# Kernel optimization log

Measured on AMD Instinct MI355X. Metric: run time of the kernel, lower is better.

## Reference

```python
import jax, jax.numpy as jnp
import numpy as np

B = 256      # number of graphs (args.batch_size)
NPG = 1000   # nodes per graph (args.num_node)
C = 64       # in_channels
DEG = 16     # avg degree
K = 500      # ceil(ratio * NPG), ratio = 0.5
EPS = 1e-8


def setup_inputs() -> dict:
    key = jax.random.key(0)
    k1, k2, k3, k4, k5 = jax.random.split(key, 5)
    N = B * NPG
    epg = NPG * DEG  # edges per graph
    x = jax.random.normal(k1, (N, C), jnp.float32)
    src = jax.random.randint(k2, (B, epg), 0, NPG)
    dst = jax.random.randint(k3, (B, epg), 0, NPG)
    off = (jnp.arange(B, dtype=jnp.int32) * NPG)[:, None]
    edge_index = jnp.stack([(src + off).reshape(-1), (dst + off).reshape(-1)]).astype(jnp.int32)
    edge_attr = jax.random.uniform(k4, (B * epg,), jnp.float32)
    batch = jnp.repeat(jnp.arange(B, dtype=jnp.int32), NPG)
    W = jax.random.normal(k5, (C, C), jnp.float32) * (1.0 / np.sqrt(C))
    b = jnp.zeros((C,), jnp.float32)
    return {"istraining": 1, "x": x, "edge_index": edge_index, "edge_attr": edge_attr,
            "batch": batch, "W": W, "b": b}


def _gcn_conv(x, edge_index, W, b):
    # PyG GCNConv: x' = D^{-1/2} (A + I) D^{-1/2} X W + b, unit edge weights.
    N = x.shape[0]
    sl = jnp.arange(N, dtype=edge_index.dtype)
    src = jnp.concatenate([edge_index[0], sl])  # message source j
    dst = jnp.concatenate([edge_index[1], sl])  # aggregation target i
    deg = jnp.zeros((N,), x.dtype).at[dst].add(1.0)
    dinv = jnp.where(deg > 0, jax.lax.rsqrt(jnp.maximum(deg, 1.0)), 0.0)
    norm = dinv[src] * dinv[dst]          # [E+N]
    h = x @ W                              # [N, C]
    msg = h[src] * norm[:, None]           # gather + scale (dominant traffic)
    out = jax.ops.segment_sum(msg, dst, num_segments=N) + b
    return out


def _node_score(x):
    # compute_node_score: cosine similarity of each node to its graph centroid
    # (community prototype), plus KL(softmax(score) || uniform) per graph.
    xb = x.reshape(B, NPG, C)
    cen = xb.mean(axis=1, keepdims=True)                       # [B,1,C]
    num = jnp.sum(xb * cen, axis=-1)                           # [B,NPG]
    den = jnp.linalg.norm(xb, axis=-1) * jnp.linalg.norm(cen, axis=-1) + EPS
    score = num / den                                          # [B,NPG]
    logp = jax.nn.log_softmax(score, axis=1)
    kl = jnp.sum(jnp.exp(logp) * (logp + jnp.log(jnp.float32(NPG))), axis=1)  # [B]
    indices_ = jnp.argsort(-score, axis=1)                     # [B,NPG]
    return score, kl, indices_


def reference(istraining, x, edge_index, edge_attr, batch, W, b):
    N = x.shape[0]
    x = _gcn_conv(x, edge_index, W, b)
    score, kl_all_batch, indices_ = _node_score(x)
    # per-graph top-k (fixed k since every graph has NPG nodes)
    _, idx = jax.lax.top_k(score, K)                           # [B,K]
    perm = ((jnp.arange(B, dtype=idx.dtype) * NPG)[:, None] + idx).reshape(-1)  # [B*K]
    score_flat = score.reshape(-1)
    x_new = x[perm] * jnp.tanh(score_flat[perm])[:, None]
    batch_new = batch[perm]
    # filter_adj: keep edges with both endpoints retained, re-index to new ids.
    mapping = jnp.full((N,), -1, dtype=jnp.int32).at[perm].set(
        jnp.arange(perm.shape[0], dtype=jnp.int32))
    new_ei = mapping[edge_index]                               # [2,E], -1 = dropped
    edge_mask = jnp.logical_and(new_ei[0] >= 0, new_ei[1] >= 0)
    edge_attr_new = jnp.where(edge_mask, edge_attr, 0.0)
    return (x_new, new_ei, edge_attr_new, edge_mask, batch_new, perm, kl_all_batch, indices_)
```

## Files before the change

### kernel.cpp

```cpp
#include <hip/hip_runtime.h>
#include <math.h>

#define NPG 1000
#define KTOP 500
#define C 64
#define EPG 16000
#define BPG 63

__device__ __forceinline__ float readlane_f(float v, int l) {
    return __uint_as_float(__builtin_amdgcn_readlane(__float_as_uint(v), (unsigned)l));
}
__device__ __forceinline__ int readlane_i(int v, int l) {
    return (int)__builtin_amdgcn_readlane((unsigned)v, (unsigned)l);
}

__global__ __launch_bounds__(1024) void build_graph_k(const int* __restrict__ ei, int E,
                                                      int* __restrict__ deg,
                                                      float* __restrict__ dinv,
                                                      int* __restrict__ off,
                                                      int* __restrict__ csr) {
    int g = blockIdx.x, t = threadIdx.x;
    __shared__ int cnt[NPG];
    __shared__ int soff[NPG];
    __shared__ unsigned short lcsr[EPG];
    __shared__ int red[1024];
    const int gbase = g * NPG;
    const int ebase = g * EPG;
    const int* __restrict__ srcp = ei + ebase;
    const int* __restrict__ dstp = ei + E + ebase;

    for (int i = t; i < NPG; i += 1024) cnt[i] = 0;
    __syncthreads();
    for (int i = t; i < EPG; i += 1024) atomicAdd(&cnt[dstp[i] - gbase], 1);
    __syncthreads();
    int v = (t < NPG) ? cnt[t] : 0;
    red[t] = v;
    __syncthreads();
    for (int o = 1; o < 1024; o <<= 1) {
        int xx = (t >= o) ? red[t - o] : 0;
        __syncthreads();
        red[t] += xx;
        __syncthreads();
    }
    if (t < NPG) soff[t] = red[t] - v;
    __syncthreads();
    for (int i = t; i < NPG; i += 1024) {
        int d = cnt[i];
        deg[gbase + i] = d;
        dinv[gbase + i] = 1.0f / sqrtf((float)(d + 1));
        off[gbase + i] = ebase + soff[i];
    }
    __syncthreads();
    for (int i = t; i < NPG; i += 1024) cnt[i] = soff[i];
    __syncthreads();
    for (int i = t; i < EPG; i += 1024) {
        int d = dstp[i] - gbase;
        int pos = atomicAdd(&cnt[d], 1);
        lcsr[pos] = (unsigned short)(srcp[i] - gbase);
    }
    __syncthreads();
    int4* co = (int4*)(csr + ebase);
    for (int i = t; i < EPG / 4; i += 1024) {
        int4 vv;
        vv.x = gbase + (int)lcsr[i * 4 + 0];
        vv.y = gbase + (int)lcsr[i * 4 + 1];
        vv.z = gbase + (int)lcsr[i * 4 + 2];
        vv.w = gbase + (int)lcsr[i * 4 + 3];
        co[i] = vv;
    }
}

__global__ __launch_bounds__(256) void gemm_k(const float* __restrict__ x,
                                              const float* __restrict__ W,
                                              const float* __restrict__ dinv,
                                              float* __restrict__ h2, int N) {
    __shared__ float sW[C * C];
    int t = threadIdx.x;
    for (int i = t; i < C * C / 4; i += 256) ((float4*)sW)[i] = ((const float4*)W)[i];
    __syncthreads();
    int r0 = blockIdx.x * 512 + t;
    int r1 = r0 + 256;
    if (r0 >= N) return;
    bool has1 = (r1 < N);
    const float4* x0 = (const float4*)(x + (size_t)r0 * C);
    const float4* x1 = (const float4*)(x + (size_t)(has1 ? r1 : r0) * C);
    float acc0[C], acc1[C];
#pragma unroll
    for (int i = 0; i < C; ++i) { acc0[i] = 0.f; acc1[i] = 0.f; }
    float4 a0 = x0[0], a1 = x1[0];
    for (int k4 = 0; k4 < 16; ++k4) {
        float4 b0, b1;
        if (k4 < 15) { b0 = x0[k4 + 1]; b1 = x1[k4 + 1]; }
        const float4* wr = (const float4*)(sW + k4 * 4 * C);
        const float* a0f = (const float*)&a0;
        const float* a1f = (const float*)&a1;
#pragma unroll
        for (int c4 = 0; c4 < 16; ++c4) {
            float4 w[4];
            w[0] = wr[c4]; w[1] = wr[16 + c4]; w[2] = wr[32 + c4]; w[3] = wr[48 + c4];
            const float* wf = (const float*)w;
#pragma unroll
            for (int j = 0; j < 4; ++j) {
                float s0 = acc0[c4 * 4 + j], s1 = acc1[c4 * 4 + j];
#pragma unroll
                for (int kk = 0; kk < 4; ++kk) {
                    float wv = wf[kk * 4 + j];
                    s0 = fmaf(a0f[kk], wv, s0);
                    s1 = fmaf(a1f[kk], wv, s1);
                }
                acc0[c4 * 4 + j] = s0; acc1[c4 * 4 + j] = s1;
            }
        }
        a0 = b0; a1 = b1;
    }
    float dv0 = dinv[r0];
    float dv1 = has1 ? dinv[r1] : 0.f;
#pragma unroll
    for (int i = 0; i < C; ++i) { acc0[i] *= dv0; acc1[i] *= dv1; }
    float4* h0 = (float4*)(h2 + (size_t)r0 * C);
#pragma unroll
    for (int q = 0; q < 16; ++q) h0[q] = ((float4*)acc0)[q];
    if (has1) {
        float4* h1 = (float4*)(h2 + (size_t)r1 * C);
#pragma unroll
        for (int q = 0; q < 16; ++q) h1[q] = ((float4*)acc1)[q];
    }
}

__global__ __launch_bounds__(256) void gather_k(const int* __restrict__ csr,
                                                const int* __restrict__ off,
                                                const int* __restrict__ deg,
                                                const float* __restrict__ h2,
                                                const float* __restrict__ dinv,
                                                const float* __restrict__ bias,
                                                float* __restrict__ out2,
                                                float* __restrict__ cen_sum,
                                                int N, int B) {
    __shared__ float cenacc[C];
    int blk = blockIdx.x;
    int wave = threadIdx.x >> 6;
    int lane = threadIdx.x & 63;
    int t = threadIdx.x;
    int g, blkin;
    if ((B & 7) == 0) {
        int xcd = blk & 7, slot = blk >> 3;
        g = (slot / BPG) * 8 + xcd;
        blkin = slot % BPG;
    } else {
        g = blk / BPG;
        blkin = blk % BPG;
    }
    if (t < C) cenacc[t] = 0.f;
    __syncthreads();

    int base = blkin * 4 + wave;
    bool active = (base < NPG / 4);
    if (active) {
        int nA = g * NPG + base;
        int nB = nA + 250, nC = nA + 500, nD = nA + 750;
        int oA = off[nA], oB = off[nB], oC = off[nC], oD = off[nD];
        int dA = deg[nA], dB = deg[nB], dC = deg[nC], dD = deg[nD];
        float diA = dinv[nA], diB = dinv[nB], diC = dinv[nC], diD = dinv[nD];
        float hA = h2[(size_t)nA * C + lane];
        float hB = h2[(size_t)nB * C + lane];
        float hC = h2[(size_t)nC * C + lane];
        float hD = h2[(size_t)nD * C + lane];
        float bv = bias[lane];
        int svA = (lane < dA) ? csr[oA + lane] : nA;
        int svB = (lane < dB) ? csr[oB + lane] : nB;
        int svC = (lane < dC) ? csr[oC + lane] : nC;
        int svD = (lane < dD) ? csr[oD + lane] : nD;
        int jmA = dA < 64 ? dA : 64;
        int jmB = dB < 64 ? dB : 64;
        int jmC = dC < 64 ? dC : 64;
        int jmD = dD < 64 ? dD : 64;
        int rA = (jmA + 3) & ~3, rB = (jmB + 3) & ~3;
        int rC = (jmC + 3) & ~3, rD = (jmD + 3) & ~3;
        int m0 = rA > rB ? rA : rB;
        int m1 = rC > rD ? rC : rD;
        int mmax = m0 > m1 ? m0 : m1;
        float aA = 0.f, aB = 0.f, aC = 0.f, aD = 0.f;
        for (int j = 0; j < mmax; j += 4) {
            if (j < rA) {
                int s0 = readlane_i(svA, j + 0), s1 = readlane_i(svA, j + 1);
                int s2 = readlane_i(svA, j + 2), s3 = readlane_i(svA, j + 3);
                float v0 = h2[(size_t)s0 * C + lane];
                float v1 = h2[(size_t)s1 * C + lane];
                float v2 = h2[(size_t)s2 * C + lane];
                float v3 = h2[(size_t)s3 * C + lane];
                aA += (v0 + v1) + (v2 + v3);
            }
            if (j < rB) {
                int s0 = readlane_i(svB, j + 0), s1 = readlane_i(svB, j + 1);
                int s2 = readlane_i(svB, j + 2), s3 = readlane_i(svB, j + 3);
                float v0 = h2[(size_t)s0 * C + lane];
                float v1 = h2[(size_t)s1 * C + lane];
                float v2 = h2[(size_t)s2 * C + lane];
                float v3 = h2[(size_t)s3 * C + lane];
                aB += (v0 + v1) + (v2 + v3);
            }
            if (j < rC) {
                int s0 = readlane_i(svC, j + 0), s1 = readlane_i(svC, j + 1);
                int s2 = readlane_i(svC, j + 2), s3 = readlane_i(svC, j + 3);
                float v0 = h2[(size_t)s0 * C + lane];
                float v1 = h2[(size_t)s1 * C + lane];
                float v2 = h2[(size_t)s2 * C + lane];
                float v3 = h2[(size_t)s3 * C + lane];
                aC += (v0 + v1) + (v2 + v3);
            }
            if (j < rD) {
                int s0 = readlane_i(svD, j + 0), s1 = readlane_i(svD, j + 1);
                int s2 = readlane_i(svD, j + 2), s3 = readlane_i(svD, j + 3);
                float v0 = h2[(size_t)s0 * C + lane];
                float v1 = h2[(size_t)s1 * C + lane];
                float v2 = h2[(size_t)s2 * C + lane];
                float v3 = h2[(size_t)s3 * C + lane];
                aD += (v0 + v1) + (v2 + v3);
            }
        }
        for (int j = 64; j < dA; ++j) aA += h2[(size_t)csr[oA + j] * C + lane];
        for (int j = 64; j < dB; ++j) aB += h2[(size_t)csr[oB + j] * C + lane];
        for (int j = 64; j < dC; ++j) aC += h2[(size_t)csr[oC + j] * C + lane];
        for (int j = 64; j < dD; ++j) aD += h2[(size_t)csr[oD + j] * C + lane];
        float cA = 1.0f - (float)(rA - jmA);
        float cB = 1.0f - (float)(rB - jmB);
        float cC = 1.0f - (float)(rC - jmC);
        float cD = 1.0f - (float)(rD - jmD);
        float resA = fmaf(diA, fmaf(cA, hA, aA), bv);
        float resB = fmaf(diB, fmaf(cB, hB, aB), bv);
        float resC = fmaf(diC, fmaf(cC, hC, aC), bv);
        float resD = fmaf(diD, fmaf(cD, hD, aD), bv);
        out2[(size_t)nA * C + lane] = resA;
        out2[(size_t)nB * C + lane] = resB;
        out2[(size_t)nC * C + lane] = resC;
        out2[(size_t)nD * C + lane] = resD;
        float csum = (resA + resB) + (resC + resD);
        atomicAdd(&cenacc[lane], csum);
    }
    __syncthreads();
    if (t < C) atomicAdd(&cen_sum[(size_t)g * C + t], cenacc[t]);
}

__global__ __launch_bounds__(1024) void post_k(const float* __restrict__ out2,
                                               const float* __restrict__ cen_sum,
                                               const int* __restrict__ ei,
                                               const float* __restrict__ eattr,
                                               float* __restrict__ o_xnew,
                                               float* __restrict__ o_newei,
                                               float* __restrict__ o_eattr,
                                               float* __restrict__ o_mask,
                                               float* __restrict__ o_batch,
                                               float* __restrict__ o_perm,
                                               float* __restrict__ o_kl,
                                               float* __restrict__ o_ind,
                                               int E) {
    __shared__ float ss[NPG];
    __shared__ float red[1024];
    __shared__ unsigned long long kk[1024];
    __shared__ int   map[NPG];
    __shared__ float cenl[C];
    __shared__ float cns;
    int g = blockIdx.x, t = threadIdx.x;
    int wave = t >> 6, lane = t & 63;
    const int gbase = g * NPG;
    const int ebase = g * EPG;

    if (t < C) cenl[t] = cen_sum[(size_t)g * C + t] * (1.0f / 1000.0f);
    __syncthreads();
    if (t < 64) {
        float m = cenl[t];
        float v = m * m;
        for (int o = 32; o > 0; o >>= 1) v += __shfl_down(v, o, 64);
        if (t == 0) cns = sqrtf(v);
    }
    __syncthreads();
    float cv = cenl[lane];
    float cn = cns;
    for (int n = wave; n < NPG; n += 16) {
        float a = out2[(size_t)(gbase + n) * C + lane];
        float num = a * cv;
        float sq = a * a;
        for (int o = 32; o > 0; o >>= 1) {
            num += __shfl_down(num, o, 64);
            sq  += __shfl_down(sq, o, 64);
        }
        if (lane == 0) ss[n] = num / (sqrtf(sq) * cn + 1e-8f);
    }
    __syncthreads();
    float mx = -INFINITY;
    for (int i = t; i < NPG; i += 1024) mx = fmaxf(mx, ss[i]);
    red[t] = mx;
    __syncthreads();
    for (int w = 512; w > 0; w >>= 1) { if (t < w) red[t] = fmaxf(red[t], red[t + w]); __syncthreads(); }
    mx = red[0];
    __syncthreads();
    float se = 0.f;
    for (int i = t; i < NPG; i += 1024) se += expf(ss[i] - mx);
    red[t] = se;
    __syncthreads();
    for (int w = 512; w > 0; w >>= 1) { if (t < w) red[t] += red[t + w]; __syncthreads(); }
    float lse = logf(red[0]);
    __syncthreads();
    float kl = 0.f;
    const float ln_npg = 6.9077552790f;
    for (int i = t; i < NPG; i += 1024) {
        float lp = ss[i] - mx - lse;
        kl += expf(lp) * (lp + ln_npg);
    }
    red[t] = kl;
    __syncthreads();
    for (int w = 512; w > 0; w >>= 1) { if (t < w) red[t] += red[t + w]; __syncthreads(); }
    if (t == 0) o_kl[g] = red[0];
    unsigned long long v;
    if (t < NPG) {
        unsigned u = __float_as_uint(ss[t]);
        u = (u & 0x80000000u) ? ~u : (u | 0x80000000u);
        v = ((unsigned long long)(~u) << 32) | (unsigned)t;
    } else {
        v = ~0ULL;
    }
    __syncthreads();
    kk[t] = v;
    __syncthreads();
    for (int k = 2; k <= 1024; k <<= 1) {
        for (int j = k >> 1; j > 0; j >>= 1) {
            int ixj = t ^ j;
            if (ixj > t) {
                unsigned long long a = kk[t], b2 = kk[ixj];
                bool up = ((t & k) == 0);
                if ((a > b2) == up) { kk[t] = b2; kk[ixj] = a; }
            }
            __syncthreads();
        }
    }
    if (t < NPG) {
        int idx = (int)(kk[t] & 0xFFFFFFFFULL);
        o_ind[(size_t)g * NPG + t] = (float)idx;
        map[t] = -1;
    }
    __syncthreads();
    if (t < KTOP) {
        int node = (int)(kk[t] & 0xFFFFFFFFULL);
        map[node] = g * KTOP + t;
        o_perm[(size_t)g * KTOP + t] = (float)(gbase + node);
        o_batch[(size_t)g * KTOP + t] = (float)g;
    }
    __syncthreads();
    for (int r = wave; r < KTOP; r += 16) {
        int node = (int)(kk[r] & 0xFFFFFFFFULL);
        float tn = tanhf(ss[node]);
        o_xnew[((size_t)g * KTOP + r) * C + lane] =
            out2[(size_t)(gbase + node) * C + lane] * tn;
    }
    const int4* src4 = (const int4*)(ei + ebase);
    const int4* dst4 = (const int4*)(ei + E + ebase);
    const float4* at4 = (const float4*)(eattr + ebase);
    float4* nei0 = (float4*)(o_newei + ebase);
    float4* nei1 = (float4*)(o_newei + E + ebase);
    float4* msk4 = (float4*)(o_mask + ebase);
    float4* eat4 = (float4*)(o_eattr + ebase);
    for (int e4 = t; e4 < EPG / 4; e4 += 1024) {
        int4 s = src4[e4], d = dst4[e4];
        int a0 = map[s.x - gbase], a1 = map[s.y - gbase];
        int a2 = map[s.z - gbase], a3 = map[s.w - gbase];
        int b0 = map[d.x - gbase], b1 = map[d.y - gbase];
        int b2 = map[d.z - gbase], b3 = map[d.w - gbase];
        float4 f0 = { (float)a0, (float)a1, (float)a2, (float)a3 };
        float4 f1 = { (float)b0, (float)b1, (float)b2, (float)b3 };
        nei0[e4] = f0;
        nei1[e4] = f1;
        float4 at = at4[e4];
        float4 mk, ea;
        mk.x = (a0 >= 0 && b0 >= 0) ? 1.0f : 0.0f;
        mk.y = (a1 >= 0 && b1 >= 0) ? 1.0f : 0.0f;
        mk.z = (a2 >= 0 && b2 >= 0) ? 1.0f : 0.0f;
        mk.w = (a3 >= 0 && b3 >= 0) ? 1.0f : 0.0f;
        ea.x = mk.x != 0.0f ? at.x : 0.0f;
        ea.y = mk.y != 0.0f ? at.y : 0.0f;
        ea.z = mk.z != 0.0f ? at.z : 0.0f;
        ea.w = mk.w != 0.0f ? at.w : 0.0f;
        msk4[e4] = mk;
        eat4[e4] = ea;
    }
}

extern "C" void kernel_launch(void* const* d_in, const int* in_sizes, int n_in,
                              void* d_out, int out_size, void* d_ws, size_t ws_size,
                              hipStream_t stream) {
    (void)n_in; (void)out_size; (void)ws_size;
    const float* x     = (const float*)d_in[1];
    const int*   ei    = (const int*)d_in[2];
    const float* eattr = (const float*)d_in[3];
    const float* W     = (const float*)d_in[5];
    const float* bias  = (const float*)d_in[6];

    const int N  = in_sizes[1] / C;
    const int E  = in_sizes[2] / 2;
    const int B  = N / NPG;
    const int BK = B * KTOP;

    char* wsp = (char*)d_ws;
    float* out2    = (float*)wsp; wsp += (size_t)N * C * 4;
    float* dinv    = (float*)wsp; wsp += (size_t)N * 4;
    int*   deg     = (int*)wsp;   wsp += (size_t)N * 4;
    int*   off     = (int*)wsp;   wsp += (size_t)N * 4;
    float* cen_sum = (float*)wsp; wsp += (size_t)B * C * 4;

    float* out     = (float*)d_out;
    float* o_xnew  = out;
    float* o_newei = o_xnew + (size_t)BK * C;
    float* o_eattr = o_newei + 2 * (size_t)E;
    float* o_mask  = o_eattr + (size_t)E;
    float* o_batch = o_mask + (size_t)E;
    float* o_perm  = o_batch + (size_t)BK;
    float* o_kl    = o_perm + (size_t)BK;
    float* o_ind   = o_kl + (size_t)B;

    float* h2buf = out;
    int*   csr   = (int*)o_eattr;

    hipMemsetAsync(cen_sum, 0, (size_t)B * C * 4, stream);

    build_graph_k<<<B, 1024, 0, stream>>>(ei, E, deg, dinv, off, csr);
    gemm_k<<<(N + 511) / 512, 256, 0, stream>>>(x, W, dinv, h2buf, N);
    gather_k<<<B * BPG, 256, 0, stream>>>(csr, off, deg, h2buf, dinv, bias, out2,
                                          cen_sum, N, B);
    post_k<<<B, 1024, 0, stream>>>(out2, cen_sum, ei, eattr,
                                   o_xnew, o_newei, o_eattr, o_mask,
                                   o_batch, o_perm, o_kl, o_ind, E);
}
```

Measured before the change: 401.2 us.

## Split graph build, co-schedule CSR scatter with GEMM, move edge filtering to grid-wide kernel

The old 1024-thread graph builder is split into a small degree-count kernel and a CSR scatter phase. The scatter phase runs in the same launch as the dense GEMM, with some blocks assigned to each role, so the serial per-graph scatter overlaps with the GEMM. The edge filtering and re-indexing moves out of the per-graph post kernel into a separate fully parallel kernel that reads a node mapping stored in global memory. The score loop also processes four nodes per wave iteration to interleave the shuffle reductions. The cost is an extra global mapping buffer and two additional kernel launches.

```diff
diff --git a/kernel.cpp b/kernel.cpp
--- a/kernel.cpp
+++ b/kernel.cpp
@@ -14,116 +14,138 @@
     return (int)__builtin_amdgcn_readlane((unsigned)v, (unsigned)l);
 }
 
-__global__ __launch_bounds__(1024) void build_graph_k(const int* __restrict__ ei, int E,
-                                                      int* __restrict__ deg,
-                                                      float* __restrict__ dinv,
-                                                      int* __restrict__ off,
-                                                      int* __restrict__ csr) {
+__global__ __launch_bounds__(256) void count_k(const int* __restrict__ ei, int E,
+                                               int* __restrict__ deg,
+                                               float* __restrict__ dinv,
+                                               int* __restrict__ off) {
     int g = blockIdx.x, t = threadIdx.x;
     __shared__ int cnt[NPG];
     __shared__ int soff[NPG];
-    __shared__ unsigned short lcsr[EPG];
-    __shared__ int red[1024];
+    __shared__ int red[256];
     const int gbase = g * NPG;
     const int ebase = g * EPG;
-    const int* __restrict__ srcp = ei + ebase;
     const int* __restrict__ dstp = ei + E + ebase;
 
-    for (int i = t; i < NPG; i += 1024) cnt[i] = 0;
-    __syncthreads();
-    for (int i = t; i < EPG; i += 1024) atomicAdd(&cnt[dstp[i] - gbase], 1);
-    __syncthreads();
-    int v = (t < NPG) ? cnt[t] : 0;
-    red[t] = v;
-    __syncthreads();
-    for (int o = 1; o < 1024; o <<= 1) {
+    for (int i = t; i < NPG; i += 256) cnt[i] = 0;
+    __syncthreads();
+    for (int i = t; i < EPG; i += 256) atomicAdd(&cnt[dstp[i] - gbase], 1);
+    __syncthreads();
+    int base = t * 4;
+    int v0 = 0, v1 = 0, v2 = 0, v3 = 0;
+    if (base + 0 < NPG) v0 = cnt[base + 0];
+    if (base + 1 < NPG) v1 = cnt[base + 1];
+    if (base + 2 < NPG) v2 = cnt[base + 2];
+    if (base + 3 < NPG) v3 = cnt[base + 3];
+    int s = v0 + v1 + v2 + v3;
+    red[t] = s;
+    __syncthreads();
+    for (int o = 1; o < 256; o <<= 1) {
         int xx = (t >= o) ? red[t - o] : 0;
         __syncthreads();
         red[t] += xx;
         __syncthreads();
     }
-    if (t < NPG) soff[t] = red[t] - v;
-    __syncthreads();
-    for (int i = t; i < NPG; i += 1024) {
+    int p = red[t] - s;
+    if (base + 0 < NPG) { soff[base + 0] = p; p += v0; }
+    if (base + 1 < NPG) { soff[base + 1] = p; p += v1; }
+    if (base + 2 < NPG) { soff[base + 2] = p; p += v2; }
+    if (base + 3 < NPG) { soff[base + 3] = p; p += v3; }
+    __syncthreads();
+    for (int i = t; i < NPG; i += 256) {
         int d = cnt[i];
         deg[gbase + i] = d;
         dinv[gbase + i] = 1.0f / sqrtf((float)(d + 1));
         off[gbase + i] = ebase + soff[i];
     }
-    __syncthreads();
-    for (int i = t; i < NPG; i += 1024) cnt[i] = soff[i];
-    __syncthreads();
-    for (int i = t; i < EPG; i += 1024) {
-        int d = dstp[i] - gbase;
-        int pos = atomicAdd(&cnt[d], 1);
-        lcsr[pos] = (unsigned short)(srcp[i] - gbase);
-    }
-    __syncthreads();
-    int4* co = (int4*)(csr + ebase);
-    for (int i = t; i < EPG / 4; i += 1024) {
-        int4 vv;
-        vv.x = gbase + (int)lcsr[i * 4 + 0];
-        vv.y = gbase + (int)lcsr[i * 4 + 1];
-        vv.z = gbase + (int)lcsr[i * 4 + 2];
-        vv.w = gbase + (int)lcsr[i * 4 + 3];
-        co[i] = vv;
-    }
-}
-
-__global__ __launch_bounds__(256) void gemm_k(const float* __restrict__ x,
-                                              const float* __restrict__ W,
-                                              const float* __restrict__ dinv,
-                                              float* __restrict__ h2, int N) {
-    __shared__ float sW[C * C];
+}
+
+__global__ __launch_bounds__(256) void scatter_gemm_k(const int* __restrict__ ei, int E,
+                                                      const int* __restrict__ off,
+                                                      int* __restrict__ csr,
+                                                      const float* __restrict__ x,
+                                                      const float* __restrict__ W,
+                                                      const float* __restrict__ dinv,
+                                                      float* __restrict__ h2,
+                                                      int N, int B) {
+    __shared__ char smem[36000] __attribute__((aligned(16)));
     int t = threadIdx.x;
-    for (int i = t; i < C * C / 4; i += 256) ((float4*)sW)[i] = ((const float4*)W)[i];
-    __syncthreads();
-    int r0 = blockIdx.x * 512 + t;
-    int r1 = r0 + 256;
-    if (r0 >= N) return;
-    bool has1 = (r1 < N);
-    const float4* x0 = (const float4*)(x + (size_t)r0 * C);
-    const float4* x1 = (const float4*)(x + (size_t)(has1 ? r1 : r0) * C);
-    float acc0[C], acc1[C];
-#pragma unroll
-    for (int i = 0; i < C; ++i) { acc0[i] = 0.f; acc1[i] = 0.f; }
-    float4 a0 = x0[0], a1 = x1[0];
-    for (int k4 = 0; k4 < 16; ++k4) {
-        float4 b0, b1;
-        if (k4 < 15) { b0 = x0[k4 + 1]; b1 = x1[k4 + 1]; }
-        const float4* wr = (const float4*)(sW + k4 * 4 * C);
-        const float* a0f = (const float*)&a0;
-        const float* a1f = (const float*)&a1;
-#pragma unroll
-        for (int c4 = 0; c4 < 16; ++c4) {
-            float4 w[4];
-            w[0] = wr[c4]; w[1] = wr[16 + c4]; w[2] = wr[32 + c4]; w[3] = wr[48 + c4];
-            const float* wf = (const float*)w;
-#pragma unroll
-            for (int j = 0; j < 4; ++j) {
-                float s0 = acc0[c4 * 4 + j], s1 = acc1[c4 * 4 + j];
-#pragma unroll
-                for (int kk = 0; kk < 4; ++kk) {
-                    float wv = wf[kk * 4 + j];
-                    s0 = fmaf(a0f[kk], wv, s0);
-                    s1 = fmaf(a1f[kk], wv, s1);
+    if (blockIdx.x < (unsigned)B) {
+        int* cnt = (int*)smem;
+        unsigned short* lcsr = (unsigned short*)(smem + 4000);
+        int g = blockIdx.x;
+        const int gbase = g * NPG;
+        const int ebase = g * EPG;
+        const int* __restrict__ srcp = ei + ebase;
+        const int* __restrict__ dstp = ei + E + ebase;
+        for (int i = t; i < NPG; i += 256) cnt[i] = off[gbase + i] - ebase;
+        __syncthreads();
+        for (int i = t; i < EPG; i += 256) {
+            int d = dstp[i] - gbase;
+            int pos = atomicAdd(&cnt[d], 1);
+            lcsr[pos] = (unsigned short)(srcp[i] - gbase);
+        }
+        __syncthreads();
+        int4* co = (int4*)(csr + ebase);
+        for (int i = t; i < EPG / 4; i += 256) {
+            int4 vv;
+            vv.x = gbase + (int)lcsr[i * 4 + 0];
+            vv.y = gbase + (int)lcsr[i * 4 + 1];
+            vv.z = gbase + (int)lcsr[i * 4 + 2];
+            vv.w = gbase + (int)lcsr[i * 4 + 3];
+            co[i] = vv;
+        }
+    } else {
+        float* sW = (float*)smem;
+        for (int i = t; i < C * C / 4; i += 256) ((float4*)sW)[i] = ((const float4*)W)[i];
+        __syncthreads();
+        int gb = blockIdx.x - B;
+        int r0 = gb * 512 + t;
+        int r1 = r0 + 256;
+        if (r0 >= N) return;
+        bool has1 = (r1 < N);
+        const float4* x0 = (const float4*)(x + (size_t)r0 * C);
+        const float4* x1 = (const float4*)(x + (size_t)(has1 ? r1 : r0) * C);
+        float acc0[C], acc1[C];
+#pragma unroll
+        for (int i = 0; i < C; ++i) { acc0[i] = 0.f; acc1[i] = 0.f; }
+        float4 a0 = x0[0], a1 = x1[0];
+        for (int k4 = 0; k4 < 16; ++k4) {
+            float4 b0, b1;
+            if (k4 < 15) { b0 = x0[k4 + 1]; b1 = x1[k4 + 1]; }
+            const float4* wr = (const float4*)(sW + k4 * 4 * C);
+            const float* a0f = (const float*)&a0;
+            const float* a1f = (const float*)&a1;
+#pragma unroll
+            for (int c4 = 0; c4 < 16; ++c4) {
+                float4 w[4];
+                w[0] = wr[c4]; w[1] = wr[16 + c4]; w[2] = wr[32 + c4]; w[3] = wr[48 + c4];
+                const float* wf = (const float*)w;
+#pragma unroll
+                for (int j = 0; j < 4; ++j) {
+                    float s0 = acc0[c4 * 4 + j], s1 = acc1[c4 * 4 + j];
+#pragma unroll
+                    for (int kk = 0; kk < 4; ++kk) {
+                        float wv = wf[kk * 4 + j];
+                        s0 = fmaf(a0f[kk], wv, s0);
+                        s1 = fmaf(a1f[kk], wv, s1);
+                    }
+                    acc0[c4 * 4 + j] = s0; acc1[c4 * 4 + j] = s1;
                 }
-                acc0[c4 * 4 + j] = s0; acc1[c4 * 4 + j] = s1;
-            }
-        }
-        a0 = b0; a1 = b1;
-    }
-    float dv0 = dinv[r0];
-    float dv1 = has1 ? dinv[r1] : 0.f;
-#pragma unroll
-    for (int i = 0; i < C; ++i) { acc0[i] *= dv0; acc1[i] *= dv1; }
-    float4* h0 = (float4*)(h2 + (size_t)r0 * C);
-#pragma unroll
-    for (int q = 0; q < 16; ++q) h0[q] = ((float4*)acc0)[q];
-    if (has1) {
-        float4* h1 = (float4*)(h2 + (size_t)r1 * C);
-#pragma unroll
-        for (int q = 0; q < 16; ++q) h1[q] = ((float4*)acc1)[q];
+            }
+            a0 = b0; a1 = b1;
+        }
+        float dv0 = dinv[r0];
+        float dv1 = has1 ? dinv[r1] : 0.f;
+#pragma unroll
+        for (int i = 0; i < C; ++i) { acc0[i] *= dv0; acc1[i] *= dv1; }
+        float4* h0 = (float4*)(h2 + (size_t)r0 * C);
+#pragma unroll
+        for (int q = 0; q < 16; ++q) h0[q] = ((float4*)acc0)[q];
+        if (has1) {
+            float4* h1 = (float4*)(h2 + (size_t)r1 * C);
+#pragma unroll
+            for (int q = 0; q < 16; ++q) h1[q] = ((float4*)acc1)[q];
+        }
     }
 }
 
@@ -241,19 +263,14 @@
     if (t < C) atomicAdd(&cen_sum[(size_t)g * C + t], cenacc[t]);
 }
 
-__global__ __launch_bounds__(1024) void post_k(const float* __restrict__ out2,
-                                               const float* __restrict__ cen_sum,
-                                               const int* __restrict__ ei,
-                                               const float* __restrict__ eattr,
-                                               float* __restrict__ o_xnew,
-                                               float* __restrict__ o_newei,
-                                               float* __restrict__ o_eattr,
-                                               float* __restrict__ o_mask,
-                                               float* __restrict__ o_batch,
-                                               float* __restrict__ o_perm,
-                                               float* __restrict__ o_kl,
-                                               float* __restrict__ o_ind,
-                                               int E) {
+__global__ __launch_bounds__(1024) void post1_k(const float* __restrict__ out2,
+                                                const float* __restrict__ cen_sum,
+                                                int* __restrict__ mapping,
+                                                float* __restrict__ o_xnew,
+                                                float* __restrict__ o_batch,
+                                                float* __restrict__ o_perm,
+                                                float* __restrict__ o_kl,
+                                                float* __restrict__ o_ind) {
     __shared__ float ss[NPG];
     __shared__ float red[1024];
     __shared__ unsigned long long kk[1024];
@@ -263,7 +280,6 @@
     int g = blockIdx.x, t = threadIdx.x;
     int wave = t >> 6, lane = t & 63;
     const int gbase = g * NPG;
-    const int ebase = g * EPG;
 
     if (t < C) cenl[t] = cen_sum[(size_t)g * C + t] * (1.0f / 1000.0f);
     __syncthreads();
@@ -276,15 +292,25 @@
     __syncthreads();
     float cv = cenl[lane];
     float cn = cns;
-    for (int n = wave; n < NPG; n += 16) {
-        float a = out2[(size_t)(gbase + n) * C + lane];
-        float num = a * cv;
-        float sq = a * a;
+    for (int base = wave * 4; base < NPG; base += 64) {
+        float a0 = out2[(size_t)(gbase + base + 0) * C + lane];
+        float a1 = out2[(size_t)(gbase + base + 1) * C + lane];
+        float a2 = out2[(size_t)(gbase + base + 2) * C + lane];
+        float a3 = out2[(size_t)(gbase + base + 3) * C + lane];
+        float n0 = a0 * cv, n1 = a1 * cv, n2 = a2 * cv, n3 = a3 * cv;
+        float q0 = a0 * a0, q1 = a1 * a1, q2 = a2 * a2, q3 = a3 * a3;
         for (int o = 32; o > 0; o >>= 1) {
-            num += __shfl_down(num, o, 64);
-            sq  += __shfl_down(sq, o, 64);
-        }
-        if (lane == 0) ss[n] = num / (sqrtf(sq) * cn + 1e-8f);
+            n0 += __shfl_down(n0, o, 64); q0 += __shfl_down(q0, o, 64);
+            n1 += __shfl_down(n1, o, 64); q1 += __shfl_down(q1, o, 64);
+            n2 += __shfl_down(n2, o, 64); q2 += __shfl_down(q2, o, 64);
+            n3 += __shfl_down(n3, o, 64); q3 += __shfl_down(q3, o, 64);
+        }
+        if (lane == 0) {
+            ss[base + 0] = n0 / (sqrtf(q0) * cn + 1e-8f);
+            ss[base + 1] = n1 / (sqrtf(q1) * cn + 1e-8f);
+            ss[base + 2] = n2 / (sqrtf(q2) * cn + 1e-8f);
+            ss[base + 3] = n3 / (sqrtf(q3) * cn + 1e-8f);
+        }
     }
     __syncthreads();
     float mx = -INFINITY;
@@ -346,30 +372,30 @@
         o_batch[(size_t)g * KTOP + t] = (float)g;
     }
     __syncthreads();
+    if (t < NPG) mapping[gbase + t] = map[t];
     for (int r = wave; r < KTOP; r += 16) {
         int node = (int)(kk[r] & 0xFFFFFFFFULL);
         float tn = tanhf(ss[node]);
         o_xnew[((size_t)g * KTOP + r) * C + lane] =
             out2[(size_t)(gbase + node) * C + lane] * tn;
     }
-    const int4* src4 = (const int4*)(ei + ebase);
-    const int4* dst4 = (const int4*)(ei + E + ebase);
-    const float4* at4 = (const float4*)(eattr + ebase);
-    float4* nei0 = (float4*)(o_newei + ebase);
-    float4* nei1 = (float4*)(o_newei + E + ebase);
-    float4* msk4 = (float4*)(o_mask + ebase);
-    float4* eat4 = (float4*)(o_eattr + ebase);
-    for (int e4 = t; e4 < EPG / 4; e4 += 1024) {
-        int4 s = src4[e4], d = dst4[e4];
-        int a0 = map[s.x - gbase], a1 = map[s.y - gbase];
-        int a2 = map[s.z - gbase], a3 = map[s.w - gbase];
-        int b0 = map[d.x - gbase], b1 = map[d.y - gbase];
-        int b2 = map[d.z - gbase], b3 = map[d.w - gbase];
+}
+
+__global__ void edge_out_k(const int* __restrict__ ei, const float* __restrict__ eattr,
+                           const int* __restrict__ mapping, float* __restrict__ o_newei,
+                           float* __restrict__ o_eattr, float* __restrict__ o_mask, int E) {
+    int e4 = blockIdx.x * 256 + threadIdx.x;
+    int q = E >> 2;
+    if (e4 < q) {
+        int4 sidx = ((const int4*)ei)[e4];
+        int4 didx = ((const int4*)ei)[q + e4];
+        int a0 = mapping[sidx.x], a1 = mapping[sidx.y], a2 = mapping[sidx.z], a3 = mapping[sidx.w];
+        int b0 = mapping[didx.x], b1 = mapping[didx.y], b2 = mapping[didx.z], b3 = mapping[didx.w];
         float4 f0 = { (float)a0, (float)a1, (float)a2, (float)a3 };
         float4 f1 = { (float)b0, (float)b1, (float)b2, (float)b3 };
-        nei0[e4] = f0;
-        nei1[e4] = f1;
-        float4 at = at4[e4];
+        ((float4*)o_newei)[e4] = f0;
+        ((float4*)o_newei)[q + e4] = f1;
+        float4 at = ((const float4*)eattr)[e4];
         float4 mk, ea;
         mk.x = (a0 >= 0 && b0 >= 0) ? 1.0f : 0.0f;
         mk.y = (a1 >= 0 && b1 >= 0) ? 1.0f : 0.0f;
@@ -379,8 +405,8 @@
         ea.y = mk.y != 0.0f ? at.y : 0.0f;
         ea.z = mk.z != 0.0f ? at.z : 0.0f;
         ea.w = mk.w != 0.0f ? at.w : 0.0f;
-        msk4[e4] = mk;
-        eat4[e4] = ea;
+        ((float4*)o_mask)[e4] = mk;
+        ((float4*)o_eattr)[e4] = ea;
     }
 }
 
@@ -404,6 +430,7 @@
     float* dinv    = (float*)wsp; wsp += (size_t)N * 4;
     int*   deg     = (int*)wsp;   wsp += (size_t)N * 4;
     int*   off     = (int*)wsp;   wsp += (size_t)N * 4;
+    int*   mapping = (int*)wsp;   wsp += (size_t)N * 4;
     float* cen_sum = (float*)wsp; wsp += (size_t)B * C * 4;
 
     float* out     = (float*)d_out;
@@ -421,11 +448,13 @@
 
     hipMemsetAsync(cen_sum, 0, (size_t)B * C * 4, stream);
 
-    build_graph_k<<<B, 1024, 0, stream>>>(ei, E, deg, dinv, off, csr);
-    gemm_k<<<(N + 511) / 512, 256, 0, stream>>>(x, W, dinv, h2buf, N);
+    count_k<<<B, 256, 0, stream>>>(ei, E, deg, dinv, off);
+    scatter_gemm_k<<<B + (N + 511) / 512, 256, 0, stream>>>(ei, E, off, csr,
+                                                            x, W, dinv, h2buf, N, B);
     gather_k<<<B * BPG, 256, 0, stream>>>(csr, off, deg, h2buf, dinv, bias, out2,
                                           cen_sum, N, B);
-    post_k<<<B, 1024, 0, stream>>>(out2, cen_sum, ei, eattr,
-                                   o_xnew, o_newei, o_eattr, o_mask,
-                                   o_batch, o_perm, o_kl, o_ind, E);
-}
+    post1_k<<<B, 1024, 0, stream>>>(out2, cen_sum, mapping,
+                                    o_xnew, o_batch, o_perm, o_kl, o_ind);
+    edge_out_k<<<(E / 4 + 255) / 256, 256, 0, stream>>>(ei, eattr, mapping,
+                                                        o_newei, o_eattr, o_mask, E);
+}
```

Result: slower. 433.0 us (+7.9%).

## Split post-processing into grid-wide score, per-graph sort, and edge filter kernels

Applied to the files above, without the earlier changes.

Breaks the monolithic per-graph post kernel, which ran only one 1024-thread block per graph, into separate stages. A centroid-finalize kernel, a grid-wide cosine-score kernel (four rows per wave), a per-graph softmax/KL/sort/top-k kernel, and a grid-wide edge remap kernel that reads a global mapping array. The intent is to spread the bandwidth-heavy score and edge phases across many more blocks so the GPU is better occupied. The cost is extra launches and global round trips for the score and mapping arrays.

```diff
diff --git a/kernel.cpp b/kernel.cpp
--- a/kernel.cpp
+++ b/kernel.cpp
@@ -7,9 +7,6 @@
 #define EPG 16000
 #define BPG 63
 
-__device__ __forceinline__ float readlane_f(float v, int l) {
-    return __uint_as_float(__builtin_amdgcn_readlane(__float_as_uint(v), (unsigned)l));
-}
 __device__ __forceinline__ int readlane_i(int v, int l) {
     return (int)__builtin_amdgcn_readlane((unsigned)v, (unsigned)l);
 }
@@ -241,71 +238,85 @@
     if (t < C) atomicAdd(&cen_sum[(size_t)g * C + t], cenacc[t]);
 }
 
-__global__ __launch_bounds__(1024) void post_k(const float* __restrict__ out2,
-                                               const float* __restrict__ cen_sum,
-                                               const int* __restrict__ ei,
-                                               const float* __restrict__ eattr,
-                                               float* __restrict__ o_xnew,
-                                               float* __restrict__ o_newei,
-                                               float* __restrict__ o_eattr,
-                                               float* __restrict__ o_mask,
-                                               float* __restrict__ o_batch,
-                                               float* __restrict__ o_perm,
-                                               float* __restrict__ o_kl,
-                                               float* __restrict__ o_ind,
-                                               int E) {
+__global__ void cen_fin_k(const float* __restrict__ cen_sum, float* __restrict__ cen,
+                          float* __restrict__ cnorm) {
+    int g = blockIdx.x, c = threadIdx.x;
+    float m = cen_sum[(size_t)g * C + c] * (1.0f / 1000.0f);
+    cen[g * C + c] = m;
+    float v = m * m;
+    for (int o = 32; o > 0; o >>= 1) v += __shfl_down(v, o, 64);
+    if (c == 0) cnorm[g] = sqrtf(v);
+}
+
+__global__ __launch_bounds__(256) void score2_k(const float* __restrict__ out2,
+                                                const float* __restrict__ cen,
+                                                const float* __restrict__ cnorm,
+                                                float* __restrict__ score, int N) {
+    int wave = threadIdx.x >> 6, lane = threadIdx.x & 63;
+    int r0 = blockIdx.x * 16 + wave * 4;
+    if (r0 >= N) return;
+    int g0 = r0 / NPG, g1 = (r0 + 1) / NPG, g2 = (r0 + 2) / NPG, g3 = (r0 + 3) / NPG;
+    float a0 = out2[(size_t)(r0 + 0) * C + lane];
+    float a1 = out2[(size_t)(r0 + 1) * C + lane];
+    float a2 = out2[(size_t)(r0 + 2) * C + lane];
+    float a3 = out2[(size_t)(r0 + 3) * C + lane];
+    float c0 = cen[g0 * C + lane];
+    float c1 = cen[g1 * C + lane];
+    float c2 = cen[g2 * C + lane];
+    float c3 = cen[g3 * C + lane];
+    float n0 = a0 * c0, n1 = a1 * c1, n2 = a2 * c2, n3 = a3 * c3;
+    float q0 = a0 * a0, q1 = a1 * a1, q2 = a2 * a2, q3 = a3 * a3;
+    for (int o = 32; o > 0; o >>= 1) {
+        n0 += __shfl_down(n0, o, 64); q0 += __shfl_down(q0, o, 64);
+        n1 += __shfl_down(n1, o, 64); q1 += __shfl_down(q1, o, 64);
+        n2 += __shfl_down(n2, o, 64); q2 += __shfl_down(q2, o, 64);
+        n3 += __shfl_down(n3, o, 64); q3 += __shfl_down(q3, o, 64);
+    }
+    if (lane == 0) {
+        score[r0 + 0] = n0 / (sqrtf(q0) * cnorm[g0] + 1e-8f);
+        score[r0 + 1] = n1 / (sqrtf(q1) * cnorm[g1] + 1e-8f);
+        score[r0 + 2] = n2 / (sqrtf(q2) * cnorm[g2] + 1e-8f);
+        score[r0 + 3] = n3 / (sqrtf(q3) * cnorm[g3] + 1e-8f);
+    }
+}
+
+__global__ __launch_bounds__(1024) void post2_k(const float* __restrict__ score,
+                                                const float* __restrict__ out2,
+                                                int* __restrict__ mapping,
+                                                float* __restrict__ o_xnew,
+                                                float* __restrict__ o_batch,
+                                                float* __restrict__ o_perm,
+                                                float* __restrict__ o_kl,
+                                                float* __restrict__ o_ind) {
     __shared__ float ss[NPG];
     __shared__ float red[1024];
     __shared__ unsigned long long kk[1024];
     __shared__ int   map[NPG];
-    __shared__ float cenl[C];
-    __shared__ float cns;
     int g = blockIdx.x, t = threadIdx.x;
     int wave = t >> 6, lane = t & 63;
     const int gbase = g * NPG;
-    const int ebase = g * EPG;
-
-    if (t < C) cenl[t] = cen_sum[(size_t)g * C + t] * (1.0f / 1000.0f);
-    __syncthreads();
-    if (t < 64) {
-        float m = cenl[t];
-        float v = m * m;
-        for (int o = 32; o > 0; o >>= 1) v += __shfl_down(v, o, 64);
-        if (t == 0) cns = sqrtf(v);
-    }
-    __syncthreads();
-    float cv = cenl[lane];
-    float cn = cns;
-    for (int n = wave; n < NPG; n += 16) {
-        float a = out2[(size_t)(gbase + n) * C + lane];
-        float num = a * cv;
-        float sq = a * a;
-        for (int o = 32; o > 0; o >>= 1) {
-            num += __shfl_down(num, o, 64);
-            sq  += __shfl_down(sq, o, 64);
-        }
-        if (lane == 0) ss[n] = num / (sqrtf(sq) * cn + 1e-8f);
-    }
+
+    const float4* s4 = (const float4*)(score + (size_t)gbase);
+    if (t < NPG / 4) ((float4*)ss)[t] = s4[t];
     __syncthreads();
     float mx = -INFINITY;
-    for (int i = t; i < NPG; i += 1024) mx = fmaxf(mx, ss[i]);
+    if (t < NPG) mx = ss[t];
     red[t] = mx;
     __syncthreads();
     for (int w = 512; w > 0; w >>= 1) { if (t < w) red[t] = fmaxf(red[t], red[t + w]); __syncthreads(); }
     mx = red[0];
     __syncthreads();
-    float se = 0.f;
-    for (int i = t; i < NPG; i += 1024) se += expf(ss[i] - mx);
+    float se = (t < NPG) ? expf(ss[t] - mx) : 0.f;
     red[t] = se;
     __syncthreads();
     for (int w = 512; w > 0; w >>= 1) { if (t < w) red[t] += red[t + w]; __syncthreads(); }
     float lse = logf(red[0]);
     __syncthreads();
+    const float ln_npg = 6.9077552790f;
     float kl = 0.f;
-    const float ln_npg = 6.9077552790f;
-    for (int i = t; i < NPG; i += 1024) {
-        float lp = ss[i] - mx - lse;
-        kl += expf(lp) * (lp + ln_npg);
+    if (t < NPG) {
+        float lp = ss[t] - mx - lse;
+        kl = expf(lp) * (lp + ln_npg);
     }
     red[t] = kl;
     __syncthreads();
@@ -346,30 +357,30 @@
         o_batch[(size_t)g * KTOP + t] = (float)g;
     }
     __syncthreads();
+    if (t < NPG) mapping[gbase + t] = map[t];
     for (int r = wave; r < KTOP; r += 16) {
         int node = (int)(kk[r] & 0xFFFFFFFFULL);
         float tn = tanhf(ss[node]);
         o_xnew[((size_t)g * KTOP + r) * C + lane] =
             out2[(size_t)(gbase + node) * C + lane] * tn;
     }
-    const int4* src4 = (const int4*)(ei + ebase);
-    const int4* dst4 = (const int4*)(ei + E + ebase);
-    const float4* at4 = (const float4*)(eattr + ebase);
-    float4* nei0 = (float4*)(o_newei + ebase);
-    float4* nei1 = (float4*)(o_newei + E + ebase);
-    float4* msk4 = (float4*)(o_mask + ebase);
-    float4* eat4 = (float4*)(o_eattr + ebase);
-    for (int e4 = t; e4 < EPG / 4; e4 += 1024) {
-        int4 s = src4[e4], d = dst4[e4];
-        int a0 = map[s.x - gbase], a1 = map[s.y - gbase];
-        int a2 = map[s.z - gbase], a3 = map[s.w - gbase];
-        int b0 = map[d.x - gbase], b1 = map[d.y - gbase];
-        int b2 = map[d.z - gbase], b3 = map[d.w - gbase];
+}
+
+__global__ void edge_out_k(const int* __restrict__ ei, const float* __restrict__ eattr,
+                           const int* __restrict__ mapping, float* __restrict__ o_newei,
+                           float* __restrict__ o_eattr, float* __restrict__ o_mask, int E) {
+    int e4 = blockIdx.x * 256 + threadIdx.x;
+    int q = E >> 2;
+    if (e4 < q) {
+        int4 sidx = ((const int4*)ei)[e4];
+        int4 didx = ((const int4*)ei)[q + e4];
+        int a0 = mapping[sidx.x], a1 = mapping[sidx.y], a2 = mapping[sidx.z], a3 = mapping[sidx.w];
+        int b0 = mapping[didx.x], b1 = mapping[didx.y], b2 = mapping[didx.z], b3 = mapping[didx.w];
         float4 f0 = { (float)a0, (float)a1, (float)a2, (float)a3 };
         float4 f1 = { (float)b0, (float)b1, (float)b2, (float)b3 };
-        nei0[e4] = f0;
-        nei1[e4] = f1;
-        float4 at = at4[e4];
+        ((float4*)o_newei)[e4] = f0;
+        ((float4*)o_newei)[q + e4] = f1;
+        float4 at = ((const float4*)eattr)[e4];
         float4 mk, ea;
         mk.x = (a0 >= 0 && b0 >= 0) ? 1.0f : 0.0f;
         mk.y = (a1 >= 0 && b1 >= 0) ? 1.0f : 0.0f;
@@ -379,8 +390,8 @@
         ea.y = mk.y != 0.0f ? at.y : 0.0f;
         ea.z = mk.z != 0.0f ? at.z : 0.0f;
         ea.w = mk.w != 0.0f ? at.w : 0.0f;
-        msk4[e4] = mk;
-        eat4[e4] = ea;
+        ((float4*)o_mask)[e4] = mk;
+        ((float4*)o_eattr)[e4] = ea;
     }
 }
 
@@ -404,7 +415,11 @@
     float* dinv    = (float*)wsp; wsp += (size_t)N * 4;
     int*   deg     = (int*)wsp;   wsp += (size_t)N * 4;
     int*   off     = (int*)wsp;   wsp += (size_t)N * 4;
+    int*   mapping = (int*)wsp;   wsp += (size_t)N * 4;
+    float* score   = (float*)wsp; wsp += (size_t)N * 4;
     float* cen_sum = (float*)wsp; wsp += (size_t)B * C * 4;
+    float* cen     = (float*)wsp; wsp += (size_t)B * C * 4;
+    float* cnorm   = (float*)wsp; wsp += 1024;
 
     float* out     = (float*)d_out;
     float* o_xnew  = out;
@@ -425,7 +440,10 @@
     gemm_k<<<(N + 511) / 512, 256, 0, stream>>>(x, W, dinv, h2buf, N);
     gather_k<<<B * BPG, 256, 0, stream>>>(csr, off, deg, h2buf, dinv, bias, out2,
                                           cen_sum, N, B);
-    post_k<<<B, 1024, 0, stream>>>(out2, cen_sum, ei, eattr,
-                                   o_xnew, o_newei, o_eattr, o_mask,
-                                   o_batch, o_perm, o_kl, o_ind, E);
-}
+    cen_fin_k<<<B, 64, 0, stream>>>(cen_sum, cen, cnorm);
+    score2_k<<<(N + 15) / 16, 256, 0, stream>>>(out2, cen, cnorm, score, N);
+    post2_k<<<B, 1024, 0, stream>>>(score, out2, mapping,
+                                    o_xnew, o_batch, o_perm, o_kl, o_ind);
+    edge_out_k<<<(E / 4 + 255) / 256, 256, 0, stream>>>(ei, eattr, mapping,
+                                                        o_newei, o_eattr, o_mask, E);
+}
```

After: 404.4 us. Within noise of the previous version (+0.8%).
